# Kernel optimization log

Measured on AMD Instinct MI355X. Metric: run time of the kernel, lower is better.

Reference implementation:

```python
import jax, jax.numpy as jnp
import numpy as np

B, N, K, D, A, V = 2, 32768, 16, 256, 64, 64


def setup_inputs() -> dict:
    key = jax.random.key(0)
    ks = jax.random.split(key, 20)
    r = lambda i, shape: jax.random.normal(ks[i], shape, jnp.float32) * 0.02
    return dict(
        x=jax.random.normal(ks[0], (B, N, D), jnp.float32),
        knn_idx=jax.random.randint(ks[1], (N, K), 0, N),
        knn_rel_pos=jax.random.normal(ks[2], (N, K, 3), jnp.float32),
        g1=jnp.ones((D,), jnp.float32), b1=jnp.zeros((D,), jnp.float32),
        g2=jnp.ones((D,), jnp.float32), b2=jnp.zeros((D,), jnp.float32),
        Wq=r(3, (D, A)), bq=jnp.zeros((A,), jnp.float32),
        Wk=r(4, (D, A)), bk=jnp.zeros((A,), jnp.float32),
        Wv=r(5, (D, V)), bv=jnp.zeros((V,), jnp.float32),
        Wo=r(6, (V, D)), bo=jnp.zeros((D,), jnp.float32),
        Wpa1=r(7, (3, A)), bpa1=jnp.zeros((A,), jnp.float32),
        Wpa2=r(8, (A, A)), bpa2=jnp.zeros((A,), jnp.float32),
        Wpv1=r(9, (3, V)), bpv1=jnp.zeros((V,), jnp.float32),
        Wpv2=r(10, (V, V)), bpv2=jnp.zeros((V,), jnp.float32),
        Ws1=r(11, (A, A)), bs1=jnp.zeros((A,), jnp.float32),
        Ws2=r(12, (A, 1)), bs2=jnp.zeros((1,), jnp.float32),
        Wf1=r(13, (D, 2 * D)), bf1=jnpp if False else jnp.zeros((2 * D,), jnp.float32),
        Wf2=r(14, (2 * D, D)), bf2=jnp.zeros((D,), jnp.float32),
    )


def _ln(t, g, b):
    m = t.mean(-1, keepdims=True)
    var = ((t - m) ** 2).mean(-1, keepdims=True)
    return (t - m) * jax.lax.rsqrt(var + 1e-5) * g + b


def reference(x, knn_idx, knn_rel_pos, g1, b1, g2, b2,
              Wq, bq, Wk, bk, Wv, bv, Wo, bo,
              Wpa1, bpa1, Wpa2, bpa2, Wpv1, bpv1, Wpv2, bpv2,
              Ws1, bs1, Ws2, bs2, Wf1, bf1, Wf2, bf2):
    scale = jnp.sqrt(jnp.float32(A))
    h = _ln(x, g1, b1)                       # [B,N,D]
    q = h @ Wq + bq                          # [B,N,A]
    k_all = h @ Wk + bk                      # [B,N,A]
    v_all = h @ Wv + bv                      # [B,N,V]
    kn = k_all[:, knn_idx]                   # gather -> [B,N,K,A]
    vn = v_all[:, knn_idx]                   # [B,N,K,V]
    ra = jax.nn.relu(knn_rel_pos @ Wpa1 + bpa1) @ Wpa2 + bpa2  # [N,K,A]
    rv = jax.nn.relu(knn_rel_pos @ Wpv1 + bpv1) @ Wpv2 + bpv2  # [N,K,V]
    t = jnp.tanh(q[:, :, None, :] - kn + ra[None])             # [B,N,K,A]
    score = (jax.nn.relu(t @ Ws1 + bs1) @ Ws2 + bs2)[..., 0]   # [B,N,K]
    attn = jax.nn.softmax(score / scale, axis=2)
    ctx = jnp.einsum('bnk,bnkv->bnv', attn, vn + rv[None])     # [B,N,V]
    x = x + ctx @ Wo + bo
    h2 = _ln(x, g2, b2)
    x = x + (jax.nn.gelu(h2 @ Wf1 + bf1, approximate=False) @ Wf2 + bf2)
    return x
```

## Files before the change

kernel.cpp:

```cpp
#include <hip/hip_runtime.h>
#include <hip/hip_bf16.h>
#include <math.h>

#define BB 2
#define NN 32768
#define KK 16
#define DD 256
#define AA 64
#define VV 64

typedef __attribute__((ext_vector_type(8))) short bf16x8;
typedef __attribute__((ext_vector_type(4))) float f32x4;
typedef __attribute__((ext_vector_type(4))) unsigned short u16x4;

__device__ __forceinline__ ushort f2bf(float v) {
  __hip_bfloat16 b = __float2bfloat16(v);
  ushort u; __builtin_memcpy(&u, &b, 2);
  return u;
}
__device__ __forceinline__ float bflo(unsigned u) { return __uint_as_float(u << 16); }
__device__ __forceinline__ float bfhi(unsigned u) { return __uint_as_float(u & 0xffff0000u); }

__device__ __forceinline__ void astore(ushort* A, int row, int col, float v) {
  int off = (row * 128 + col * 2) ^ ((row & 7) << 4);
  *reinterpret_cast<ushort*>(reinterpret_cast<char*>(A) + off) = f2bf(v);
}
__device__ __forceinline__ bf16x8 afrag(const ushort* A, int rowbase, int lane, int ks) {
  int row = rowbase + (lane & 15), g = lane >> 4;
  int off = (row * 128 + ks * 64 + g * 16) ^ ((row & 7) << 4);
  return *reinterpret_cast<const bf16x8*>(reinterpret_cast<const char*>(A) + off);
}
__device__ __forceinline__ bf16x8 loadfrag(const ushort* p, int fi, int lane) {
  return *reinterpret_cast<const bf16x8*>(&p[((size_t)fi * 64 + lane) * 8]);
}

__global__ __launch_bounds__(256) void k_prep(
    const float* __restrict__ Wq, const float* __restrict__ Wk, const float* __restrict__ Wv,
    const float* __restrict__ Wf1, const float* __restrict__ Wf2,
    const float* __restrict__ Wpa2, const float* __restrict__ Wpv2,
    const float* __restrict__ Ws1, const float* __restrict__ Wo,
    const float* __restrict__ Wpa1, const float* __restrict__ Wpv1,
    ushort* __restrict__ pQKV, ushort* __restrict__ pWf1, ushort* __restrict__ pWf2,
    ushort* __restrict__ pS, ushort* __restrict__ pWo) {
  int tid = blockIdx.x * 256 + threadIdx.x;
  int lane = tid & 63, g = lane >> 4, c16 = lane & 15;
  bf16x8 f;
  if (tid < 6144) {
    int fi = tid >> 6; int ks = fi / 12, nt = fi % 12;
    int col = nt * 16 + c16;
    const float* W = (col < 64) ? Wq : (col < 128) ? Wk : Wv;
    int c = col & 63;
#pragma unroll
    for (int e = 0; e < 8; e++) f[e] = (short)f2bf(W[(ks * 32 + g * 8 + e) * 64 + c]);
    *reinterpret_cast<bf16x8*>(&pQKV[(size_t)tid * 8]) = f;
  } else if (tid < 22528) {
    int t2 = tid - 6144; int fi = t2 >> 6; int ks = fi >> 5, nt = fi & 31;
    int col = nt * 16 + c16;
#pragma unroll
    for (int e = 0; e < 8; e++) f[e] = (short)f2bf(Wf1[(ks * 32 + g * 8 + e) * 512 + col]);
    *reinterpret_cast<bf16x8*>(&pWf1[(size_t)t2 * 8]) = f;
  } else if (tid < 38912) {
    int t3 = tid - 22528; int fi = t3 >> 6; int ks = fi >> 4, nt = fi & 15;
    int col = nt * 16 + c16;
#pragma unroll
    for (int e = 0; e < 8; e++) f[e] = (short)f2bf(Wf2[(ks * 32 + g * 8 + e) * 256 + col]);
    *reinterpret_cast<bf16x8*>(&pWf2[(size_t)t3 * 8]) = f;
  } else if (tid < 40960) {
    int t4 = tid - 38912; int fi = t4 >> 6;
    if (fi < 24) {
      int mat = fi >> 3, ks = (fi >> 2) & 1, nt = fi & 3;
      const float* W = (mat == 0) ? Wpa2 : (mat == 1) ? Wpv2 : Ws1;
      int col = nt * 16 + c16;
#pragma unroll
      for (int e = 0; e < 8; e++) f[e] = (short)f2bf(W[(ks * 32 + g * 8 + e) * 64 + col]);
    } else {
      int mat = (fi - 24) >> 2, nt = fi & 3;
      const float* W = mat ? Wpv1 : Wpa1;
      int col = nt * 16 + c16;
#pragma unroll
      for (int e = 0; e < 8; e++) {
        int K = g * 8 + e;
        f[e] = (K < 3) ? (short)f2bf(W[K * 64 + col]) : (short)0;
      }
    }
    *reinterpret_cast<bf16x8*>(&pS[(size_t)t4 * 8]) = f;
  } else if (tid < 43008) {
    int t5 = tid - 40960; int fi = t5 >> 6; int ks = fi >> 4, nt = fi & 15;
    int col = nt * 16 + c16;
#pragma unroll
    for (int e = 0; e < 8; e++) f[e] = (short)f2bf(Wo[(ks * 32 + g * 8 + e) * 256 + col]);
    *reinterpret_cast<bf16x8*>(&pWo[(size_t)t5 * 8]) = f;
  }
}

__global__ __launch_bounds__(256) void k_qkv(
    const float* __restrict__ x, const float* __restrict__ g1, const float* __restrict__ b1,
    const ushort* __restrict__ pW,
    const float* __restrict__ bq, const float* __restrict__ bk, const float* __restrict__ bv,
    ushort* __restrict__ qo, ushort* __restrict__ ko, ushort* __restrict__ vo) {
  __shared__ __align__(16) ushort hs[32 * 256];
  int t = threadIdx.x, lane = t & 63, w = t >> 6;
  size_t row0 = (size_t)blockIdx.x * 32;

  {
    const float4 gv = *reinterpret_cast<const float4*>(&g1[lane * 4]);
    const float4 bvv = *reinterpret_cast<const float4*>(&b1[lane * 4]);
#pragma unroll
    for (int r8 = 0; r8 < 8; r8++) {
      int r = w * 8 + r8;
      const float4 xv = *reinterpret_cast<const float4*>(&x[(row0 + r) * DD + lane * 4]);
      float s = xv.x + xv.y + xv.z + xv.w;
      float s2 = xv.x * xv.x + xv.y * xv.y + xv.z * xv.z + xv.w * xv.w;
      for (int o = 32; o > 0; o >>= 1) { s += __shfl_down(s, o, 64); s2 += __shfl_down(s2, o, 64); }
      s = __shfl(s, 0, 64); s2 = __shfl(s2, 0, 64);
      float m = s * (1.f / DD), rs = rsqrtf(s2 * (1.f / DD) - m * m + 1e-5f);
      u16x4 hv;
      hv[0] = f2bf((xv.x - m) * rs * gv.x + bvv.x);
      hv[1] = f2bf((xv.y - m) * rs * gv.y + bvv.y);
      hv[2] = f2bf((xv.z - m) * rs * gv.z + bvv.z);
      hv[3] = f2bf((xv.w - m) * rs * gv.w + bvv.w);
      int off = (r * 512 + lane * 8) ^ ((r & 7) << 4);
      *reinterpret_cast<u16x4*>(reinterpret_cast<char*>(hs) + off) = hv;
    }
  }
  __syncthreads();

  f32x4 acc[2][3] = {};
  bf16x8 fw[3][3];
  int rowa = lane & 15, gg = lane >> 4;
#pragma unroll
  for (int p = 0; p < 2; p++)
#pragma unroll
    for (int j = 0; j < 3; j++) fw[p][j] = loadfrag(pW, p * 12 + w * 3 + j, lane);
#pragma unroll
  for (int ks = 0; ks < 8; ks++) {
    if (ks + 2 < 8) {
#pragma unroll
      for (int j = 0; j < 3; j++) fw[(ks + 2) % 3][j] = loadfrag(pW, (ks + 2) * 12 + w * 3 + j, lane);
    }
    bf16x8 a0 = *reinterpret_cast<const bf16x8*>(reinterpret_cast<const char*>(hs) +
                 ((rowa * 512 + ks * 64 + gg * 16) ^ ((rowa & 7) << 4)));
    bf16x8 a1 = *reinterpret_cast<const bf16x8*>(reinterpret_cast<const char*>(hs) +
                 (((rowa + 16) * 512 + ks * 64 + gg * 16) ^ ((rowa & 7) << 4)));
#pragma unroll
    for (int j = 0; j < 3; j++) {
      acc[0][j] = __builtin_amdgcn_mfma_f32_16x16x32_bf16(a0, fw[ks % 3][j], acc[0][j], 0, 0, 0);
      acc[1][j] = __builtin_amdgcn_mfma_f32_16x16x32_bf16(a1, fw[ks % 3][j], acc[1][j], 0, 0, 0);
    }
  }

#pragma unroll
  for (int j = 0; j < 3; j++) {
    int ntg = w * 3 + j;
    int buf = ntg >> 2;
    ushort* out = (buf == 0) ? qo : (buf == 1) ? ko : vo;
    const float* bias = (buf == 0) ? bq : (buf == 1) ? bk : bv;
    int col = (ntg & 3) * 16 + (lane & 15);
    float bb = bias[col];
#pragma unroll
    for (int mt = 0; mt < 2; mt++)
#pragma unroll
      for (int r = 0; r < 4; r++) {
        int row = mt * 16 + (lane >> 4) * 4 + r;
        out[(row0 + row) * 64 + col] = f2bf(acc[mt][j][r] + bb);
      }
  }
}

__global__ __launch_bounds__(256) void k_attn(
    const float* __restrict__ x, const float* __restrict__ relpos, const int* __restrict__ knn,
    const ushort* __restrict__ qg, const ushort* __restrict__ kg, const ushort* __restrict__ vg,
    const float* __restrict__ bpa1, const float* __restrict__ bpa2,
    const float* __restrict__ bpv1, const float* __restrict__ bpv2,
    const ushort* __restrict__ pS, const float* __restrict__ bs1,
    const float* __restrict__ Ws2, const float* __restrict__ bs2,
    const ushort* __restrict__ pWo, const float* __restrict__ bo,
    float* __restrict__ xmid) {
  int n0 = blockIdx.x * 2;
  int t = threadIdx.x, lane = t & 63, w = t >> 6;
  int g = lane >> 4, c16 = lane & 15;
  int col = w * 16 + c16;

  __shared__ __align__(16) ushort A0[64 * 64];
  __shared__ __align__(16) ushort TT[64 * 64];
  __shared__ __align__(16) ushort hid_bs[64][72];
  __shared__ __align__(16) ushort RP[32 * 32];
  __shared__ __align__(16) ushort ctile[16 * 64];
  __shared__ float attn_s[64];
  __shared__ int idx_s[2][16];

  if (t < 32) {
    idx_s[t >> 4][t & 15] = knn[(n0 + (t >> 4)) * KK + (t & 15)];
    float r0 = relpos[(size_t)n0 * 48 + t * 3 + 0];
    float r1 = relpos[(size_t)n0 * 48 + t * 3 + 1];
    float r2 = relpos[(size_t)n0 * 48 + t * 3 + 2];
    uint4 z; z.x = 0; z.y = 0; z.z = 0; z.w = 0;
    uint4 f0;
    f0.x = ((unsigned)f2bf(r1) << 16) | (unsigned)f2bf(r0);
    f0.y = (unsigned)f2bf(r2);
    f0.z = 0; f0.w = 0;
    *reinterpret_cast<uint4*>(&RP[t * 32 + 0])  = f0;
    *reinterpret_cast<uint4*>(&RP[t * 32 + 8])  = z;
    *reinterpret_cast<uint4*>(&RP[t * 32 + 16]) = z;
    *reinterpret_cast<uint4*>(&RP[t * 32 + 24]) = z;
  }
  __syncthreads();

  ushort ku[2][2][4];
  float qf[2][2];
#pragma unroll
  for (int pt = 0; pt < 2; pt++)
#pragma unroll
    for (int b = 0; b < 2; b++) {
      qf[pt][b] = bflo((unsigned)qg[((size_t)b * NN + n0 + pt) * AA + col]);
#pragma unroll
      for (int r = 0; r < 4; r++)
        ku[pt][b][r] = kg[((size_t)b * NN + idx_s[pt][g * 4 + r]) * AA + col];
    }

  {
    bf16x8 aRP0 = *reinterpret_cast<const bf16x8*>(&RP[(lane & 15) * 32 + g * 8]);
    bf16x8 aRP1 = *reinterpret_cast<const bf16x8*>(&RP[((lane & 15) + 16) * 32 + g * 8]);
    bf16x8 bA = loadfrag(pS, 24 + w, lane);
    bf16x8 bV = loadfrag(pS, 28 + w, lane);
    float ba = bpa1[col], bv1_ = bpv1[col];
    f32x4 zz = {0.f, 0.f, 0.f, 0.f};
    f32x4 hA0 = __builtin_amdgcn_mfma_f32_16x16x32_bf16(aRP0, bA, zz, 0, 0, 0);
    f32x4 hA1 = __builtin_amdgcn_mfma_f32_16x16x32_bf16(aRP1, bA, zz, 0, 0, 0);
    f32x4 hV0 = __builtin_amdgcn_mfma_f32_16x16x32_bf16(aRP0, bV, zz, 0, 0, 0);
    f32x4 hV1 = __builtin_amdgcn_mfma_f32_16x16x32_bf16(aRP1, bV, zz, 0, 0, 0);
#pragma unroll
    for (int r = 0; r < 4; r++) {
      astore(A0, 0  + g * 4 + r, col, fmaxf(hA0[r] + ba, 0.f));
      astore(A0, 16 + g * 4 + r, col, fmaxf(hA1[r] + ba, 0.f));
      astore(A0, 32 + g * 4 + r, col, fmaxf(hV0[r] + bv1_, 0.f));
      astore(A0, 48 + g * 4 + r, col, fmaxf(hV1[r] + bv1_, 0.f));
    }
  }
  __syncthreads();

  float ra_reg[2][4], rv_reg[2][4];
  {
    bf16x8 bwa0 = loadfrag(pS, 0 + w, lane);
    bf16x8 bwa1 = loadfrag(pS, 4 + w, lane);
    bf16x8 bwv0 = loadfrag(pS, 8 + w, lane);
    bf16x8 bwv1 = loadfrag(pS, 12 + w, lane);
    float ba2 = bpa2[col], bv2 = bpv2[col];
#pragma unroll
    for (int mt = 0; mt < 2; mt++) {
      bf16x8 a0 = afrag(A0, mt * 16, lane, 0), a1 = afrag(A0, mt * 16, lane, 1);
      f32x4 acc = {0.f, 0.f, 0.f, 0.f};
      acc = __builtin_amdgcn_mfma_f32_16x16x32_bf16(a0, bwa0, acc, 0, 0, 0);
      acc = __builtin_amdgcn_mfma_f32_16x16x32_bf16(a1, bwa1, acc, 0, 0, 0);
#pragma unroll
      for (int r = 0; r < 4; r++) ra_reg[mt][r] = acc[r] + ba2;
      bf16x8 v0 = afrag(A0, 32 + mt * 16, lane, 0), v1 = afrag(A0, 32 + mt * 16, lane, 1);
      f32x4 accv = {0.f, 0.f, 0.f, 0.f};
      accv = __builtin_amdgcn_mfma_f32_16x16x32_bf16(v0, bwv0, accv, 0, 0, 0);
      accv = __builtin_amdgcn_mfma_f32_16x16x32_bf16(v1, bwv1, accv, 0, 0, 0);
#pragma unroll
      for (int r = 0; r < 4; r++) rv_reg[mt][r] = accv[r] + bv2;
    }
  }

#pragma unroll
  for (int pt = 0; pt < 2; pt++)
#pragma unroll
    for (int b = 0; b < 2; b++)
#pragma unroll
      for (int r = 0; r < 4; r++) {
        float kf = bflo((unsigned)ku[pt][b][r]);
        float xv = qf[pt][b] - kf + ra_reg[pt][r];
        float tv = 1.f - 2.f * __builtin_amdgcn_rcpf(__expf(2.f * xv) + 1.f);
        astore(TT, (pt * 2 + b) * 16 + g * 4 + r, col, tv);
      }
  __syncthreads();

  {
    bf16x8 fsA = loadfrag(pS, 16 + w, lane);
    bf16x8 fsB = loadfrag(pS, 20 + w, lane);
    float bsc = bs1[col], wsc = Ws2[col];
#pragma unroll
    for (int mt = 0; mt < 4; mt++) {
      bf16x8 a0 = afrag(TT, mt * 16, lane, 0), a1 = afrag(TT, mt * 16, lane, 1);
      f32x4 acc = {0.f, 0.f, 0.f, 0.f};
      acc = __builtin_amdgcn_mfma_f32_16x16x32_bf16(a0, fsA, acc, 0, 0, 0);
      acc = __builtin_amdgcn_mfma_f32_16x16x32_bf16(a1, fsB, acc, 0, 0, 0);
#pragma unroll
      for (int r = 0; r < 4; r++)
        hid_bs[mt * 16 + g * 4 + r][col] = f2bf(fmaxf(acc[r] + bsc, 0.f) * wsc);
    }
  }
  __syncthreads();

  if (t < 64) {
    const uint4* hrow = reinterpret_cast<const uint4*>(&hid_bs[t][0]);
    float s = 0.f;
#pragma unroll
    for (int c = 0; c < 8; c++) {
      uint4 v4 = hrow[c];
      s += bflo(v4.x) + bfhi(v4.x) + bflo(v4.y) + bfhi(v4.y) +
           bflo(v4.z) + bfhi(v4.z) + bflo(v4.w) + bfhi(v4.w);
    }
    float sc = (s + bs2[0]) * 0.125f;
    float mx = sc;
#pragma unroll
    for (int o = 8; o > 0; o >>= 1) mx = fmaxf(mx, __shfl_xor(mx, o, 64));
    float e = __expf(sc - mx);
    float ss = e;
#pragma unroll
    for (int o = 8; o > 0; o >>= 1) ss += __shfl_xor(ss, o, 64);
    attn_s[t] = e / ss;
  }
  __syncthreads();

  {
    float cacc[4] = {0.f, 0.f, 0.f, 0.f};
#pragma unroll
    for (int pt = 0; pt < 2; pt++)
#pragma unroll
      for (int b = 0; b < 2; b++) {
        int mt = pt * 2 + b;
        size_t bbase = (size_t)b * NN;
#pragma unroll
        for (int r = 0; r < 4; r++) {
          int k = g * 4 + r;
          float vf = bflo((unsigned)vg[(bbase + idx_s[pt][k]) * VV + col]);
          cacc[mt] += attn_s[mt * 16 + k] * (vf + rv_reg[pt][r]);
        }
      }
#pragma unroll
    for (int mt = 0; mt < 4; mt++) {
      cacc[mt] += __shfl_xor(cacc[mt], 16, 64);
      cacc[mt] += __shfl_xor(cacc[mt], 32, 64);
    }
    if (g == 0) {
#pragma unroll
      for (int mt = 0; mt < 4; mt++) astore(ctile, mt, col, cacc[mt]);
    }
  }
  __syncthreads();

  {
    bf16x8 a0 = afrag(ctile, 0, lane, 0), a1 = afrag(ctile, 0, lane, 1);
    f32x4 acc[4];
#pragma unroll
    for (int j = 0; j < 4; j++) {
      bf16x8 b0 = loadfrag(pWo, 0 + w * 4 + j, lane);
      bf16x8 b1 = loadfrag(pWo, 16 + w * 4 + j, lane);
      f32x4 a = {0.f, 0.f, 0.f, 0.f};
      a = __builtin_amdgcn_mfma_f32_16x16x32_bf16(a0, b0, a, 0, 0, 0);
      a = __builtin_amdgcn_mfma_f32_16x16x32_bf16(a1, b1, a, 0, 0, 0);
      acc[j] = a;
    }
    if (g == 0) {
#pragma unroll
      for (int j = 0; j < 4; j++) {
        int oc = w * 64 + j * 16 + c16;
        float bb = bo[oc];
#pragma unroll
        for (int r = 0; r < 4; r++) {
          int pt = r >> 1, b = r & 1;
          size_t addr = ((size_t)b * NN + n0 + pt) * DD + oc;
          xmid[addr] = x[addr] + acc[j][r] + bb;
        }
      }
    }
  }
}

__global__ __launch_bounds__(256) void k_ffn(
    const float* __restrict__ xmid, const float* __restrict__ g2, const float* __restrict__ b2,
    const ushort* __restrict__ pWf1, const float* __restrict__ bf1,
    const ushort* __restrict__ pWf2, const float* __restrict__ bf2,
    float* __restrict__ out) {
  __shared__ __align__(16) ushort hs[32 * 256];
  __shared__ __align__(16) ushort ys[32 * 512];
  int t = threadIdx.x, lane = t & 63, w = t >> 6;
  size_t row0 = (size_t)blockIdx.x * 32;
  int rowa = lane & 15, gg = lane >> 4;

  {
    const float4 gv = *reinterpret_cast<const float4*>(&g2[lane * 4]);
    const float4 bvv = *reinterpret_cast<const float4*>(&b2[lane * 4]);
#pragma unroll
    for (int r8 = 0; r8 < 8; r8++) {
      int r = w * 8 + r8;
      const float4 xv = *reinterpret_cast<const float4*>(&xmid[(row0 + r) * DD + lane * 4]);
      float s = xv.x + xv.y + xv.z + xv.w;
      float s2 = xv.x * xv.x + xv.y * xv.y + xv.z * xv.z + xv.w * xv.w;
      for (int o = 32; o > 0; o >>= 1) { s += __shfl_down(s, o, 64); s2 += __shfl_down(s2, o, 64); }
      s = __shfl(s, 0, 64); s2 = __shfl(s2, 0, 64);
      float m = s * (1.f / DD), rs = rsqrtf(s2 * (1.f / DD) - m * m + 1e-5f);
      u16x4 hv;
      hv[0] = f2bf((xv.x - m) * rs * gv.x + bvv.x);
      hv[1] = f2bf((xv.y - m) * rs * gv.y + bvv.y);
      hv[2] = f2bf((xv.z - m) * rs * gv.z + bvv.z);
      hv[3] = f2bf((xv.w - m) * rs * gv.w + bvv.w);
      int off = (r * 512 + lane * 8) ^ ((r & 7) << 4);
      *reinterpret_cast<u16x4*>(reinterpret_cast<char*>(hs) + off) = hv;
    }
  }
  __syncthreads();

  f32x4 acc1[2][8] = {};
  {
    bf16x8 fA[8], fB[8];
#pragma unroll
    for (int j = 0; j < 8; j++) fA[j] = loadfrag(pWf1, w * 8 + j, lane);
#pragma unroll
    for (int ks = 0; ks < 8; ks += 2) {
#pragma unroll
      for (int j = 0; j < 8; j++) fB[j] = loadfrag(pWf1, (ks + 1) * 32 + w * 8 + j, lane);
      {
        bf16x8 a0 = *reinterpret_cast<const bf16x8*>(reinterpret_cast<const char*>(hs) +
                     ((rowa * 512 + ks * 64 + gg * 16) ^ ((rowa & 7) << 4)));
        bf16x8 a1 = *reinterpret_cast<const bf16x8*>(reinterpret_cast<const char*>(hs) +
                     (((rowa + 16) * 512 + ks * 64 + gg * 16) ^ ((rowa & 7) << 4)));
#pragma unroll
        for (int j = 0; j < 8; j++) {
          acc1[0][j] = __builtin_amdgcn_mfma_f32_16x16x32_bf16(a0, fA[j], acc1[0][j], 0, 0, 0);
          acc1[1][j] = __builtin_amdgcn_mfma_f32_16x16x32_bf16(a1, fA[j], acc1[1][j], 0, 0, 0);
        }
      }
      if (ks + 2 < 8) {
#pragma unroll
        for (int j = 0; j < 8; j++) fA[j] = loadfrag(pWf1, (ks + 2) * 32 + w * 8 + j, lane);
      }
      {
        bf16x8 a0 = *reinterpret_cast<const bf16x8*>(reinterpret_cast<const char*>(hs) +
                     ((rowa * 512 + (ks + 1) * 64 + gg * 16) ^ ((rowa & 7) << 4)));
        bf16x8 a1 = *reinterpret_cast<const bf16x8*>(reinterpret_cast<const char*>(hs) +
                     (((rowa + 16) * 512 + (ks + 1) * 64 + gg * 16) ^ ((rowa & 7) << 4)));
#pragma unroll
        for (int j = 0; j < 8; j++) {
          acc1[0][j] = __builtin_amdgcn_mfma_f32_16x16x32_bf16(a0, fB[j], acc1[0][j], 0, 0, 0);
          acc1[1][j] = __builtin_amdgcn_mfma_f32_16x16x32_bf16(a1, fB[j], acc1[1][j], 0, 0, 0);
        }
      }
    }
  }

#pragma unroll
  for (int j = 0; j < 8; j++) {
    int col = w * 128 + j * 16 + (lane & 15);
    float bb = bf1[col];
#pragma unroll
    for (int mt = 0; mt < 2; mt++)
#pragma unroll
      for (int r = 0; r < 4; r++) {
        float v = acc1[mt][j][r] + bb;
        v = v * 0.5f * (1.f + erff(v * 0.70710678118654752f));
        int row = mt * 16 + (lane >> 4) * 4 + r;
        int off = (row * 1024 + col * 2) ^ ((row & 7) << 4);
        *reinterpret_cast<ushort*>(reinterpret_cast<char*>(ys) + off) = f2bf(v);
      }
  }
  __syncthreads();

  f32x4 acc2[2][4] = {};
  {
    bf16x8 f2[3][4];
#pragma unroll
    for (int p = 0; p < 2; p++)
#pragma unroll
      for (int j = 0; j < 4; j++) f2[p][j] = loadfrag(pWf2, p * 16 + w * 4 + j, lane);
#pragma unroll
    for (int ks = 0; ks < 16; ks++) {
      if (ks + 2 < 16) {
#pragma unroll
        for (int j = 0; j < 4; j++) f2[(ks + 2) % 3][j] = loadfrag(pWf2, (ks + 2) * 16 + w * 4 + j, lane);
      }
      bf16x8 a0 = *reinterpret_cast<const bf16x8*>(reinterpret_cast<const char*>(ys) +
                   ((rowa * 1024 + ks * 64 + gg * 16) ^ ((rowa & 7) << 4)));
      bf16x8 a1 = *reinterpret_cast<const bf16x8*>(reinterpret_cast<const char*>(ys) +
                   (((rowa + 16) * 1024 + ks * 64 + gg * 16) ^ ((rowa & 7) << 4)));
#pragma unroll
      for (int j = 0; j < 4; j++) {
        acc2[0][j] = __builtin_amdgcn_mfma_f32_16x16x32_bf16(a0, f2[ks % 3][j], acc2[0][j], 0, 0, 0);
        acc2[1][j] = __builtin_amdgcn_mfma_f32_16x16x32_bf16(a1, f2[ks % 3][j], acc2[1][j], 0, 0, 0);
      }
    }
  }

#pragma unroll
  for (int j = 0; j < 4; j++) {
    int col = w * 64 + j * 16 + (lane & 15);
    float bb = bf2[col];
#pragma unroll
    for (int mt = 0; mt < 2; mt++)
#pragma unroll
      for (int r = 0; r < 4; r++) {
        int row = mt * 16 + (lane >> 4) * 4 + r;
        size_t idx = (row0 + row) * DD + col;
        out[idx] = xmid[idx] + acc2[mt][j][r] + bb;
      }
  }
}

extern "C" void kernel_launch(void* const* d_in, const int* in_sizes, int n_in,
                              void* d_out, int out_size, void* d_ws, size_t ws_size,
                              hipStream_t stream) {
  const float* x      = (const float*)d_in[0];
  const int*   knn    = (const int*)  d_in[1];
  const float* relpos = (const float*)d_in[2];
  const float* g1     = (const float*)d_in[3];
  const float* b1     = (const float*)d_in[4];
  const float* g2     = (const float*)d_in[5];
  const float* b2     = (const float*)d_in[6];
  const float* Wq     = (const float*)d_in[7];
  const float* bq     = (const float*)d_in[8];
  const float* Wk     = (const float*)d_in[9];
  const float* bk     = (const float*)d_in[10];
  const float* Wv     = (const float*)d_in[11];
  const float* bv     = (const float*)d_in[12];
  const float* Wo     = (const float*)d_in[13];
  const float* bo     = (const float*)d_in[14];
  const float* Wpa1   = (const float*)d_in[15];
  const float* bpa1   = (const float*)d_in[16];
  const float* Wpa2   = (const float*)d_in[17];
  const float* bpa2   = (const float*)d_in[18];
  const float* Wpv1   = (const float*)d_in[19];
  const float* bpv1   = (const float*)d_in[20];
  const float* Wpv2   = (const float*)d_in[21];
  const float* bpv2   = (const float*)d_in[22];
  const float* Ws1    = (const float*)d_in[23];
  const float* bs1    = (const float*)d_in[24];
  const float* Ws2    = (const float*)d_in[25];
  const float* bs2    = (const float*)d_in[26];
  const float* Wf1    = (const float*)d_in[27];
  const float* bf1    = (const float*)d_in[28];
  const float* Wf2    = (const float*)d_in[29];
  const float* bf2    = (const float*)d_in[30];

  ushort* qb = (ushort*)d_ws;
  ushort* kb = qb + (size_t)BB * NN * AA;
  ushort* vb = kb + (size_t)BB * NN * AA;
  float* xmid = (float*)(vb + (size_t)BB * NN * VV);
  ushort* pQKV = (ushort*)(xmid + (size_t)BB * NN * DD);
  ushort* pWf1 = pQKV + 49152;
  ushort* pWf2 = pWf1 + 131072;
  ushort* pS   = pWf2 + 131072;
  ushort* pWo  = pS + 16384;

  k_prep<<<168, 256, 0, stream>>>(Wq, Wk, Wv, Wf1, Wf2, Wpa2, Wpv2, Ws1, Wo, Wpa1, Wpv1,
                                  pQKV, pWf1, pWf2, pS, pWo);
  k_qkv<<<(BB * NN) / 32, 256, 0, stream>>>(x, g1, b1, pQKV, bq, bk, bv, qb, kb, vb);
  k_attn<<<NN / 2, 256, 0, stream>>>(x, relpos, knn, qb, kb, vb,
                                     bpa1, bpa2, bpv1, bpv2,
                                     pS, bs1, Ws2, bs2, pWo, bo, xmid);
  k_ffn<<<(BB * NN) / 32, 256, 0, stream>>>(xmid, g2, b2, pWf1, bf1, pWf2, bf2, (float*)d_out);
}
```

Before: 421.7 us.

## Split FFN first GEMM into two halves to cut LDS and register use

The FFN kernel now computes the 512-wide hidden layer in two 256-column halves. The first half goes into a new 16KB buffer, and the second half overwrites the LayerNorm input buffer after a barrier. This halves live accumulators and cuts LDS from 48KB to 32KB per block, with launch_bounds(256,5) asking for higher occupancy. In exchange the first GEMM's A operand is read twice from LDS, and the extra sequencing plus register caps could cause spills.

```diff
diff --git a/kernel.cpp b/kernel.cpp
--- a/kernel.cpp
+++ b/kernel.cpp
@@ -369,13 +369,13 @@
   }
 }
 
-__global__ __launch_bounds__(256) void k_ffn(
+__global__ __launch_bounds__(256, 5) void k_ffn(
     const float* __restrict__ xmid, const float* __restrict__ g2, const float* __restrict__ b2,
     const ushort* __restrict__ pWf1, const float* __restrict__ bf1,
     const ushort* __restrict__ pWf2, const float* __restrict__ bf2,
     float* __restrict__ out) {
   __shared__ __align__(16) ushort hs[32 * 256];
-  __shared__ __align__(16) ushort ys[32 * 512];
+  __shared__ __align__(16) ushort ya[32 * 256];
   int t = threadIdx.x, lane = t & 63, w = t >> 6;
   size_t row0 = (size_t)blockIdx.x * 32;
   int rowa = lane & 15, gg = lane >> 4;
@@ -403,29 +403,29 @@
   }
   __syncthreads();
 
-  f32x4 acc1[2][8] = {};
-  {
-    bf16x8 fA[8], fB[8];
-#pragma unroll
-    for (int j = 0; j < 8; j++) fA[j] = loadfrag(pWf1, w * 8 + j, lane);
+  {
+    f32x4 acc[2][4] = {};
+    bf16x8 fA[4], fB[4];
+#pragma unroll
+    for (int j = 0; j < 4; j++) fA[j] = loadfrag(pWf1, w * 4 + j, lane);
 #pragma unroll
     for (int ks = 0; ks < 8; ks += 2) {
 #pragma unroll
-      for (int j = 0; j < 8; j++) fB[j] = loadfrag(pWf1, (ks + 1) * 32 + w * 8 + j, lane);
+      for (int j = 0; j < 4; j++) fB[j] = loadfrag(pWf1, (ks + 1) * 32 + w * 4 + j, lane);
       {
         bf16x8 a0 = *reinterpret_cast<const bf16x8*>(reinterpret_cast<const char*>(hs) +
                      ((rowa * 512 + ks * 64 + gg * 16) ^ ((rowa & 7) << 4)));
         bf16x8 a1 = *reinterpret_cast<const bf16x8*>(reinterpret_cast<const char*>(hs) +
                      (((rowa + 16) * 512 + ks * 64 + gg * 16) ^ ((rowa & 7) << 4)));
 #pragma unroll
-        for (int j = 0; j < 8; j++) {
-          acc1[0][j] = __builtin_amdgcn_mfma_f32_16x16x32_bf16(a0, fA[j], acc1[0][j], 0, 0, 0);
-          acc1[1][j] = __builtin_amdgcn_mfma_f32_16x16x32_bf16(a1, fA[j], acc1[1][j], 0, 0, 0);
+        for (int j = 0; j < 4; j++) {
+          acc[0][j] = __builtin_amdgcn_mfma_f32_16x16x32_bf16(a0, fA[j], acc[0][j], 0, 0, 0);
+          acc[1][j] = __builtin_amdgcn_mfma_f32_16x16x32_bf16(a1, fA[j], acc[1][j], 0, 0, 0);
         }
       }
       if (ks + 2 < 8) {
 #pragma unroll
-        for (int j = 0; j < 8; j++) fA[j] = loadfrag(pWf1, (ks + 2) * 32 + w * 8 + j, lane);
+        for (int j = 0; j < 4; j++) fA[j] = loadfrag(pWf1, (ks + 2) * 32 + w * 4 + j, lane);
       }
       {
         bf16x8 a0 = *reinterpret_cast<const bf16x8*>(reinterpret_cast<const char*>(hs) +
@@ -433,65 +433,136 @@
         bf16x8 a1 = *reinterpret_cast<const bf16x8*>(reinterpret_cast<const char*>(hs) +
                      (((rowa + 16) * 512 + (ks + 1) * 64 + gg * 16) ^ ((rowa & 7) << 4)));
 #pragma unroll
-        for (int j = 0; j < 8; j++) {
-          acc1[0][j] = __builtin_amdgcn_mfma_f32_16x16x32_bf16(a0, fB[j], acc1[0][j], 0, 0, 0);
-          acc1[1][j] = __builtin_amdgcn_mfma_f32_16x16x32_bf16(a1, fB[j], acc1[1][j], 0, 0, 0);
-        }
-      }
-    }
-  }
-
-#pragma unroll
-  for (int j = 0; j < 8; j++) {
-    int col = w * 128 + j * 16 + (lane & 15);
+        for (int j = 0; j < 4; j++) {
+          acc[0][j] = __builtin_amdgcn_mfma_f32_16x16x32_bf16(a0, fB[j], acc[0][j], 0, 0, 0);
+          acc[1][j] = __builtin_amdgcn_mfma_f32_16x16x32_bf16(a1, fB[j], acc[1][j], 0, 0, 0);
+        }
+      }
+    }
+#pragma unroll
+    for (int j = 0; j < 4; j++) {
+      int col = w * 64 + j * 16 + rowa;
+      float bb = bf1[col];
+#pragma unroll
+      for (int mt = 0; mt < 2; mt++)
+#pragma unroll
+        for (int r = 0; r < 4; r++) {
+          float v = acc[mt][j][r] + bb;
+          v = v * 0.5f * (1.f + erff(v * 0.70710678118654752f));
+          int row = mt * 16 + gg * 4 + r;
+          int off = (row * 512 + col * 2) ^ ((row & 7) << 4);
+          *reinterpret_cast<ushort*>(reinterpret_cast<char*>(ya) + off) = f2bf(v);
+        }
+    }
+  }
+
+  f32x4 accB[2][4] = {};
+  {
+    bf16x8 fA[4], fB[4];
+#pragma unroll
+    for (int j = 0; j < 4; j++) fA[j] = loadfrag(pWf1, 16 + w * 4 + j, lane);
+#pragma unroll
+    for (int ks = 0; ks < 8; ks += 2) {
+#pragma unroll
+      for (int j = 0; j < 4; j++) fB[j] = loadfrag(pWf1, (ks + 1) * 32 + 16 + w * 4 + j, lane);
+      {
+        bf16x8 a0 = *reinterpret_cast<const bf16x8*>(reinterpret_cast<const char*>(hs) +
+                     ((rowa * 512 + ks * 64 + gg * 16) ^ ((rowa & 7) << 4)));
+        bf16x8 a1 = *reinterpret_cast<const bf16x8*>(reinterpret_cast<const char*>(hs) +
+                     (((rowa + 16) * 512 + ks * 64 + gg * 16) ^ ((rowa & 7) << 4)));
+#pragma unroll
+        for (int j = 0; j < 4; j++) {
+          accB[0][j] = __builtin_amdgcn_mfma_f32_16x16x32_bf16(a0, fA[j], accB[0][j], 0, 0, 0);
+          accB[1][j] = __builtin_amdgcn_mfma_f32_16x16x32_bf16(a1, fA[j], accB[1][j], 0, 0, 0);
+        }
+      }
+      if (ks + 2 < 8) {
+#pragma unroll
+        for (int j = 0; j < 4; j++) fA[j] = loadfrag(pWf1, (ks + 2) * 32 + 16 + w * 4 + j, lane);
+      }
+      {
+        bf16x8 a0 = *reinterpret_cast<const bf16x8*>(reinterpret_cast<const char*>(hs) +
+                     ((rowa * 512 + (ks + 1) * 64 + gg * 16) ^ ((rowa & 7) << 4)));
+        bf16x8 a1 = *reinterpret_cast<const bf16x8*>(reinterpret_cast<const char*>(hs) +
+                     (((rowa + 16) * 512 + (ks + 1) * 64 + gg * 16) ^ ((rowa & 7) << 4)));
+#pragma unroll
+        for (int j = 0; j < 4; j++) {
+          accB[0][j] = __builtin_amdgcn_mfma_f32_16x16x32_bf16(a0, fB[j], accB[0][j], 0, 0, 0);
+          accB[1][j] = __builtin_amdgcn_mfma_f32_16x16x32_bf16(a1, fB[j], accB[1][j], 0, 0, 0);
+        }
+      }
+    }
+  }
+  __syncthreads();
+
+#pragma unroll
+  for (int j = 0; j < 4; j++) {
+    int col = 256 + w * 64 + j * 16 + rowa;
     float bb = bf1[col];
 #pragma unroll
     for (int mt = 0; mt < 2; mt++)
 #pragma unroll
       for (int r = 0; r < 4; r++) {
-        float v = acc1[mt][j][r] + bb;
+        float v = accB[mt][j][r] + bb;
         v = v * 0.5f * (1.f + erff(v * 0.70710678118654752f));
-        int row = mt * 16 + (lane >> 4) * 4 + r;
-        int off = (row * 1024 + col * 2) ^ ((row & 7) << 4);
-        *reinterpret_cast<ushort*>(reinterpret_cast<char*>(ys) + off) = f2bf(v);
+        int row = mt * 16 + gg * 4 + r;
+        int off = (row * 512 + (col - 256) * 2) ^ ((row & 7) << 4);
+        *reinterpret_cast<ushort*>(reinterpret_cast<char*>(hs) + off) = f2bf(v);
       }
   }
   __syncthreads();
 
   f32x4 acc2[2][4] = {};
   {
-    bf16x8 f2[3][4];
-#pragma unroll
-    for (int p = 0; p < 2; p++)
-#pragma unroll
-      for (int j = 0; j < 4; j++) f2[p][j] = loadfrag(pWf2, p * 16 + w * 4 + j, lane);
-#pragma unroll
-    for (int ks = 0; ks < 16; ks++) {
+    bf16x8 f2A[4], f2B[4];
+#pragma unroll
+    for (int j = 0; j < 4; j++) f2A[j] = loadfrag(pWf2, w * 4 + j, lane);
+#pragma unroll
+    for (int ks = 0; ks < 16; ks += 2) {
+#pragma unroll
+      for (int j = 0; j < 4; j++) f2B[j] = loadfrag(pWf2, (ks + 1) * 16 + w * 4 + j, lane);
+      {
+        const ushort* buf = (ks < 8) ? ya : hs;
+        int kl = ks & 7;
+        bf16x8 a0 = *reinterpret_cast<const bf16x8*>(reinterpret_cast<const char*>(buf) +
+                     ((rowa * 512 + kl * 64 + gg * 16) ^ ((rowa & 7) << 4)));
+        bf16x8 a1 = *reinterpret_cast<const bf16x8*>(reinterpret_cast<const char*>(buf) +
+                     (((rowa + 16) * 512 + kl * 64 + gg * 16) ^ ((rowa & 7) << 4)));
+#pragma unroll
+        for (int j = 0; j < 4; j++) {
+          acc2[0][j] = __builtin_amdgcn_mfma_f32_16x16x32_bf16(a0, f2A[j], acc2[0][j], 0, 0, 0);
+          acc2[1][j] = __builtin_amdgcn_mfma_f32_16x16x32_bf16(a1, f2A[j], acc2[1][j], 0, 0, 0);
+        }
+      }
       if (ks + 2 < 16) {
 #pragma unroll
-        for (int j = 0; j < 4; j++) f2[(ks + 2) % 3][j] = loadfrag(pWf2, (ks + 2) * 16 + w * 4 + j, lane);
-      }
-      bf16x8 a0 = *reinterpret_cast<const bf16x8*>(reinterpret_cast<const char*>(ys) +
-                   ((rowa * 1024 + ks * 64 + gg * 16) ^ ((rowa & 7) << 4)));
-      bf16x8 a1 = *reinterpret_cast<const bf16x8*>(reinterpret_cast<const char*>(ys) +
-                   (((rowa + 16) * 1024 + ks * 64 + gg * 16) ^ ((rowa & 7) << 4)));
-#pragma unroll
-      for (int j = 0; j < 4; j++) {
-        acc2[0][j] = __builtin_amdgcn_mfma_f32_16x16x32_bf16(a0, f2[ks % 3][j], acc2[0][j], 0, 0, 0);
-        acc2[1][j] = __builtin_amdgcn_mfma_f32_16x16x32_bf16(a1, f2[ks % 3][j], acc2[1][j], 0, 0, 0);
+        for (int j = 0; j < 4; j++) f2A[j] = loadfrag(pWf2, (ks + 2) * 16 + w * 4 + j, lane);
+      }
+      {
+        const ushort* buf = ((ks + 1) < 8) ? ya : hs;
+        int kl = (ks + 1) & 7;
+        bf16x8 a0 = *reinterpret_cast<const bf16x8*>(reinterpret_cast<const char*>(buf) +
+                     ((rowa * 512 + kl * 64 + gg * 16) ^ ((rowa & 7) << 4)));
+        bf16x8 a1 = *reinterpret_cast<const bf16x8*>(reinterpret_cast<const char*>(buf) +
+                     (((rowa + 16) * 512 + kl * 64 + gg * 16) ^ ((rowa & 7) << 4)));
+#pragma unroll
+        for (int j = 0; j < 4; j++) {
+          acc2[0][j] = __builtin_amdgcn_mfma_f32_16x16x32_bf16(a0, f2B[j], acc2[0][j], 0, 0, 0);
+          acc2[1][j] = __builtin_amdgcn_mfma_f32_16x16x32_bf16(a1, f2B[j], acc2[1][j], 0, 0, 0);
+        }
       }
     }
   }
 
 #pragma unroll
   for (int j = 0; j < 4; j++) {
-    int col = w * 64 + j * 16 + (lane & 15);
+    int col = w * 64 + j * 16 + rowa;
     float bb = bf2[col];
 #pragma unroll
     for (int mt = 0; mt < 2; mt++)
 #pragma unroll
       for (int r = 0; r < 4; r++) {
-        int row = mt * 16 + (lane >> 4) * 4 + r;
+        int row = mt * 16 + gg * 4 + r;
         size_t idx = (row0 + row) * DD + col;
         out[idx] = xmid[idx] + acc2[mt][j][r] + bb;
       }
```

After: 462.9 us. 9.8% more time.
